# Kernel tuning notes

Measured on AMD Instinct MI355X. Metric: run time of the kernel, lower is better.

The kernel has to match this reference:

```python
import jax, jax.numpy as jnp
import numpy as np

UNITS = 128; NRBF = 10; MAXN = 3; MAXL = 3; SBF = MAXN * MAXL
NLAYERS = 3; CUTOFF = 5.0; TB_CUTOFF = 4.0; NELEM = 95
NTOTAL = 60000; NLOCAL = 50000; NGHOST = NTOTAL - NLOCAL
NEDGE = 250000; NTRIPLE = 1000000


def silu(x):
    return x * jax.nn.sigmoid(x)


def polynomial(r, cutoff):
    # smooth polynomial cutoff, zero beyond `cutoff`
    ratio = r / cutoff
    p = 1.0 - 6.0 * ratio**5 + 15.0 * ratio**4 - 10.0 * ratio**3
    return jnp.where(r <= cutoff, p, 0.0)


def rbf(r):  # [E] -> [E, NRBF] radial basis
    mu = jnp.linspace(0.0, CUTOFF, NRBF).astype(r.dtype)
    return jnp.exp(-((r[:, None] - mu) ** 2) / 0.5)


def sbf(r, theta):  # [T],[T] -> [T, SBF] radial x angular product basis
    n = jnp.arange(1, MAXN + 1, dtype=r.dtype)
    rad = jnp.sin(n * jnp.pi * r[:, None] / TB_CUTOFF) / (r[:, None] + 1e-6)  # [T,MAXN]
    l = jnp.arange(MAXL, dtype=r.dtype)
    ang = jnp.cos(l * theta[:, None])  # [T,MAXL]
    return (rad[:, :, None] * ang[:, None, :]).reshape(r.shape[0], SBF)


def setup_inputs() -> dict:
    key = jax.random.key(0)
    ks = jax.random.split(key, 40)
    w = lambda i, shape: 0.05 * jax.random.normal(ks[i], shape, dtype=jnp.float32)
    return {
        "atomic_numbers": jax.random.randint(ks[0], (NTOTAL,), 0, NELEM),
        "atom_pos": 10.0 * jax.random.uniform(ks[1], (NTOTAL, 3), dtype=jnp.float32),
        "cell": jax.random.normal(ks[2], (1, 3, 3), dtype=jnp.float32),
        "pbc_offsets": jnp.zeros((NEDGE, 3), jnp.float32),
        "edge_src": jax.random.randint(ks[3], (NEDGE,), 0, NLOCAL),
        "edge_dst": jax.random.randint(ks[4], (NEDGE,), 0, NTOTAL),
        "three_body_indices": jax.random.randint(ks[5], (NTRIPLE, 2), 0, NEDGE),
        "batch": jnp.zeros((NTOTAL,), jnp.int32),
        "ghost_map": jax.random.randint(ks[6], (NGHOST,), 0, NLOCAL),
        "nlocal": NLOCAL,
        "atom_embed_w": w(7, (NELEM, UNITS)),
        "edge_enc_w": w(8, (NRBF, UNITS)),
        "edge_enc_b": w(9, (UNITS,)),
        "tb_atom_w": w(10, (NLAYERS, UNITS, SBF)),
        "tb_atom_b": w(11, (NLAYERS, SBF)),
        "tb_gate_w": w(12, (NLAYERS, SBF, UNITS)),
        "tb_gate_b": w(13, (NLAYERS, UNITS)),
        "ge_wm": w(14, (NLAYERS, 3 * UNITS, UNITS)),
        "ge_bm": w(15, (NLAYERS, UNITS)),
        "ge_wg": w(16, (NLAYERS, 3 * UNITS, UNITS)),
        "ge_bg": w(17, (NLAYERS, UNITS)),
        "el_edge_w": w(18, (NLAYERS, NRBF, UNITS)),
        "el_edge_b": w(19, (NLAYERS, UNITS)),
        "ga_wm": w(20, (NLAYERS, 3 * UNITS, UNITS)),
        "ga_bm": w(21, (NLAYERS, UNITS)),
        "ga_wg": w(22, (NLAYERS, 3 * UNITS, UNITS)),
        "ga_bg": w(23, (NLAYERS, UNITS)),
        "el_atom_w": w(24, (NLAYERS, NRBF, UNITS)),
        "el_atom_b": w(25, (NLAYERS, UNITS)),
        "final_w1": w(26, (UNITS, UNITS)),
        "final_b1": w(27, (UNITS,)),
        "final_w2": w(28, (UNITS, 1)),
        "final_b2": w(29, (1,)),
        "e_scale": 1.0 + w(30, (NELEM,)),
        "e_shift": w(31, (NELEM,)),
    }


def m3gnet_forward(atom_pos, cell, pbc_offsets, atom_embed_w, edge_enc_w, edge_enc_b,
                   tb_atom_w, tb_atom_b, tb_gate_w, tb_gate_b,
                   ge_wm, ge_bm, ge_wg, ge_bg, el_edge_w, el_edge_b,
                   ga_wm, ga_bm, ga_wg, ga_bg, el_atom_w, el_atom_b,
                   final_w1, final_b1, final_w2, final_b2, e_scale, e_shift,
                   atomic_numbers, edge_src, edge_dst, three_body_indices, batch, ghost_map, nlocal):
    src, dst = edge_src, edge_dst
    edge_batch = batch[src]
    # geometry
    edge_vector = atom_pos[src] - (atom_pos[dst] + jnp.einsum('bi,bij->bj', pbc_offsets, cell[edge_batch]))
    edge_length = jnp.linalg.norm(edge_vector, axis=1)  # [E]
    ij = three_body_indices[:, 0]
    ik = three_body_indices[:, 1]
    vij, vik = edge_vector[ij], edge_vector[ik]
    rij, rik = edge_length[ij], edge_length[ik]
    cos_jik = jnp.clip(jnp.sum(vij * vik, axis=1) / (rij * rik + 1e-12), -1.0 + 1e-7, 1.0 - 1e-7)
    # embeddings / bases
    atom_attr = jax.nn.one_hot(atomic_numbers, NELEM, dtype=atom_embed_w.dtype) @ atom_embed_w  # [ntotal,U]
    edge_attr_zero = rbf(edge_length)  # [E,NRBF]
    edge_attr = edge_attr_zero @ edge_enc_w + edge_enc_b  # [E,U]
    three_basis = sbf(rik, jnp.arccos(cos_jik))  # [T,SBF]
    n_edges = edge_attr.shape[0]
    cut_ij = polynomial(edge_length[ij], TB_CUTOFF)[:, None]
    cut_ik = polynomial(edge_length[ik], TB_CUTOFF)[:, None]
    center_of_k = src[ik]  # center atom of edge k (< nlocal)
    for L in range(NLAYERS):
        if L > 0:
            # LammpsExchange: pad + fill ghost slots from mapped local atoms
            atom_attr = jnp.concatenate([atom_attr, atom_attr[ghost_map]], axis=0)
        # three-body interaction
        atom_mlp_out = jax.nn.sigmoid(atom_attr[:nlocal] @ tb_atom_w[L] + tb_atom_b[L])  # [nlocal,SBF]
        atom_mask = atom_mlp_out[center_of_k] * cut_ij * cut_ik  # [T,SBF]
        tb_masked = three_basis * atom_mask
        tb_out = jnp.zeros((n_edges, SBF), tb_masked.dtype).at[ij].add(tb_masked)
        edge_attr = edge_attr + (tb_out @ tb_gate_w[L] + tb_gate_b[L])
        # edge update: gated MLP on [h_src, h_dst, e]
        feat = jnp.concatenate([atom_attr[src], atom_attr[dst], edge_attr], axis=1)  # [E,3U]
        gmlp_e = silu(feat @ ge_wm[L] + ge_bm[L]) * jax.nn.sigmoid(feat @ ge_wg[L] + ge_bg[L])
        edge_attr = edge_attr + gmlp_e * (edge_attr_zero @ el_edge_w[L] + el_edge_b[L])
        # atom update: gated MLP + scatter-add to local centers
        feat = jnp.concatenate([atom_attr[src], atom_attr[dst], edge_attr], axis=1)
        ap = silu(feat @ ga_wm[L] + ga_bm[L]) * jax.nn.sigmoid(feat @ ga_wg[L] + ga_bg[L])
        ap = ap * (edge_attr_zero @ el_atom_w[L] + el_atom_b[L])
        agg = jnp.zeros((nlocal, UNITS), ap.dtype).at[src].add(ap)
        atom_attr = atom_attr[:nlocal] + agg  # truncate ghosts
    # readout on local atoms only
    e = (silu(atom_attr @ final_w1 + final_b1) @ final_w2 + final_b2).reshape(-1)
    z_local = atomic_numbers[:nlocal]
    e = e * e_scale[z_local] + e_shift[z_local]
    return jnp.sum(e)[None]  # [1]


def reference(atomic_numbers, atom_pos, cell, pbc_offsets, edge_src, edge_dst, three_body_indices,
              batch, ghost_map, nlocal, atom_embed_w, edge_enc_w, edge_enc_b,
              tb_atom_w, tb_atom_b, tb_gate_w, tb_gate_b,
              ge_wm, ge_bm, ge_wg, ge_bg, el_edge_w, el_edge_b,
              ga_wm, ga_bm, ga_wg, ga_bg, el_atom_w, el_atom_b,
              final_w1, final_b1, final_w2, final_b2, e_scale, e_shift):
    return m3gnet_forward(atom_pos, cell, pbc_offsets, atom_embed_w, edge_enc_w, edge_enc_b,
                          tb_atom_w, tb_atom_b, tb_gate_w, tb_gate_b,
                          ge_wm, ge_bm, ge_wg, ge_bg, el_edge_w, el_edge_b,
                          ga_wm, ga_bm, ga_wg, ga_bg, el_atom_w, el_atom_b,
                          final_w1, final_b1, final_w2, final_b2, e_scale, e_shift,
                          atomic_numbers, edge_src, edge_dst, three_body_indices, batch, ghost_map, nlocal)
```

## Files before the change

kernel.cpp:

```cpp
#include <hip/hip_runtime.h>
#include <math.h>

#define UNITS   128
#define NRBF    10
#define SBF     9
#define NLAYERS 3
#define NELEM   95
#define NTOTAL  60000
#define NLOCAL  50000
#define NGHOST  10000
#define NEDGE   250000
#define NTRIPLE 1000000
#define CUTOFF  5.0f
#define TBCUT   4.0f
#define PI_F    3.14159265358979323846f
#define FSTR    424
#define MEDGE   64
#define SCHUNK  1024
#define NCHUNK  ((NEDGE + SCHUNK - 1)/SCHUNK)

typedef __attribute__((ext_vector_type(8))) short short8;
typedef __attribute__((ext_vector_type(4))) float f32x4;

__device__ __forceinline__ float sigm(float x){ return 1.0f/(1.0f+__expf(-x)); }
__device__ __forceinline__ float polycut(float r){
    float q = r*(1.0f/TBCUT);
    float q2 = q*q, q3 = q2*q;
    float p = 1.0f - 6.0f*q2*q3 + 15.0f*q2*q2 - 10.0f*q3;
    return (r <= TBCUT) ? p : 0.0f;
}
__device__ __forceinline__ ushort f2bf(float x){
    unsigned u = __float_as_uint(x);
    unsigned r = (u + 0x7fffu + ((u>>16)&1u)) >> 16;
    return (ushort)r;
}
__device__ __forceinline__ float bf2f(ushort h){
    return __uint_as_float(((unsigned)h) << 16);
}
__device__ __forceinline__ f32x4 splat4(float x){ f32x4 v = {x,x,x,x}; return v; }
__device__ __forceinline__ float gatef(float xm, float xg){
    float d = (1.0f+__expf(-xm))*(1.0f+__expf(-xg));
    return xm*__builtin_amdgcn_rcpf(d);
}

__global__ void k_edge_geom(const float* __restrict__ pos, const float* __restrict__ cell,
                            const float* __restrict__ pbc, const int* __restrict__ src,
                            const int* __restrict__ dst, const int* __restrict__ batch,
                            float* __restrict__ evec, float* __restrict__ elen,
                            float* __restrict__ rbf0){
    int e = blockIdx.x*blockDim.x + threadIdx.x;
    if (e >= NEDGE) return;
    int s = src[e], d = dst[e];
    int b = batch[s];
    const float* C = cell + b*9;
    float p0 = pbc[e*3+0], p1 = pbc[e*3+1], p2 = pbc[e*3+2];
    float vx = pos[s*3+0] - (pos[d*3+0] + p0*C[0] + p1*C[3] + p2*C[6]);
    float vy = pos[s*3+1] - (pos[d*3+1] + p0*C[1] + p1*C[4] + p2*C[7]);
    float vz = pos[s*3+2] - (pos[d*3+2] + p0*C[2] + p1*C[5] + p2*C[8]);
    float r = sqrtf(vx*vx + vy*vy + vz*vz);
    evec[e*3+0] = vx; evec[e*3+1] = vy; evec[e*3+2] = vz;
    elen[e] = r;
    #pragma unroll
    for (int i = 0; i < NRBF; i++){
        float mu = (CUTOFF/(NRBF-1))*i;
        float dm = r - mu;
        rbf0[e*NRBF + i] = __expf(-dm*dm*2.0f);
    }
}

__global__ void k_embed(const int* __restrict__ anum, const float* __restrict__ embw,
                        ushort* __restrict__ Ah){
    int t = blockIdx.x*blockDim.x + threadIdx.x;
    if (t >= NTOTAL*32) return;
    int a = t >> 5, q = t & 31;
    float4 v = ((const float4*)embw)[anum[a]*32 + q];
    ushort4 h;
    h.x = f2bf(v.x); h.y = f2bf(v.y); h.z = f2bf(v.z); h.w = f2bf(v.w);
    ((ushort4*)Ah)[t] = h;
}

__global__ void k_pack_all(const float* __restrict__ gewm, const float* __restrict__ gewg,
                           const float* __restrict__ gawm, const float* __restrict__ gawg,
                           const float* __restrict__ tbg,  const float* __restrict__ encw,
                           const float* __restrict__ elew, const float* __restrict__ elaw,
                           const float* __restrict__ gebm, const float* __restrict__ gebg,
                           const float* __restrict__ tbb,  const float* __restrict__ encb,
                           ushort* __restrict__ wmain, ushort* __restrict__ wext,
                           ushort* __restrict__ waux,  ushort* __restrict__ wencb,
                           float* __restrict__ btot){
    int blk = blockIdx.x, tid = threadIdx.x;
    if (blk < 288){
        int t = blk*256 + tid;
        if (t >= 3*4*12*8*64) return;
        int lane = t & 63;
        int nt   = (t>>6) & 7;
        int rest = t >> 9;
        int kb   = rest % 12;
        int r2   = rest / 12;
        int mat  = r2 & 3;
        int L    = r2 >> 2;
        const float* src;
        if      (mat == 0) src = gewm;
        else if (mat == 1) src = gewg;
        else if (mat == 2) src = gawm;
        else               src = gawg;
        src += (size_t)L*384*128;
        int n = nt*16 + (lane & 15);
        int kbase = kb*32 + (lane>>4)*8;
        ushort* dst = wmain + (size_t)t*8;
        #pragma unroll
        for (int j = 0; j < 8; j++) dst[j] = f2bf(src[(size_t)(kbase+j)*128 + n]);
    } else if (blk < 300){
        int t = (blk-288)*256 + tid;
        if (t >= 3*2*512) return;
        int lane = t & 63;
        int nt   = (t>>6) & 7;
        int mat  = (t>>9) & 1;
        int L    = t >> 10;
        const float* W  = ((mat==0)? gewm : gewg) + (size_t)L*384*128;
        const float* tg = tbg + (size_t)L*SBF*UNITS;
        int n = nt*16 + (lane & 15);
        ushort* dst = wext + (size_t)t*8;
        #pragma unroll
        for (int j = 0; j < 8; j++){
            int k = (lane>>4)*8 + j;
            float v = 0.0f;
            if (k >= 10 && k <= 18){
                int s = k - 10;
                for (int kk = 0; kk < 128; kk++)
                    v = fmaf(tg[s*UNITS+kk], W[(size_t)(256+kk)*128 + n], v);
            } else if (k < 10 && L == 0){
                for (int kk = 0; kk < 128; kk++)
                    v = fmaf(encw[k*UNITS+kk], W[(size_t)(256+kk)*128 + n], v);
            }
            dst[j] = f2bf(v);
        }
    } else if (blk < 318){
        int t = (blk-300)*256 + tid;
        if (t >= 3*3*512) return;
        int lane = t & 63;
        int nt   = (t>>6) & 7;
        int rest = t >> 9;
        int mat  = rest % 3;
        int L    = rest / 3;
        int n = nt*16 + (lane & 15);
        ushort* dst = waux + (size_t)t*8;
        #pragma unroll
        for (int j = 0; j < 8; j++){
            int k = (lane>>4)*8 + j;
            float v = 0.0f;
            if (mat == 0){ if (k < 10) v = elew[(size_t)L*NRBF*UNITS + k*UNITS + n]; }
            else if (mat == 1){ if (k < 10) v = elaw[(size_t)L*NRBF*UNITS + k*UNITS + n]; }
            else { if (k >= 10 && k <= 18) v = tbg[(size_t)L*SBF*UNITS + (k-10)*UNITS + n]; }
            dst[j] = f2bf(v);
        }
    } else if (blk < 320){
        int t = (blk-318)*256 + tid;
        if (t >= 512) return;
        int lane = t & 63;
        int nt   = t >> 6;
        int n = nt*16 + (lane & 15);
        ushort* dst = wencb + (size_t)t*8;
        #pragma unroll
        for (int j = 0; j < 8; j++){
            int k = (lane>>4)*8 + j;
            float v = (k < 10) ? encw[k*UNITS + n] : 0.0f;
            dst[j] = f2bf(v);
        }
    } else {
        int t = (blk-320)*256 + tid;
        if (t >= 3*2*128) return;
        int n = t & 127;
        int mat = (t>>7) & 1;
        int L = t >> 8;
        const float* W = ((mat==0)? gewm : gewg) + (size_t)L*384*128;
        const float* be = ((mat==0)? gebm : gebg) + (size_t)L*UNITS;
        const float* tb = tbb + (size_t)L*UNITS;
        float v = be[n];
        for (int kk = 0; kk < 128; kk++){
            float f = tb[kk];
            if (L == 0) f += encb[kk];
            v = fmaf(f, W[(size_t)(256+kk)*128 + n], v);
        }
        btot[t] = v;
    }
}

template<int GATHER, int WAH>
__global__ void k_tb_mlp(const float* __restrict__ Fin, const int* __restrict__ anum,
                         const float* __restrict__ embw,
                         const float* __restrict__ W, const float* __restrict__ b,
                         float* __restrict__ out, float* __restrict__ aggOut,
                         ushort* __restrict__ Ah){
    int a = blockIdx.x*blockDim.x + threadIdx.x;
    if (a >= NLOCAL) return;
    float acc[SBF];
    #pragma unroll
    for (int s = 0; s < SBF; s++) acc[s] = b[s];
    const float4* row4 = GATHER ? (const float4*)(embw + (size_t)anum[a]*UNITS)
                                : (const float4*)(Fin + (size_t)a*UNITS);
    float4* agg4 = (float4*)(aggOut + (size_t)a*UNITS);
    ushort4* ah4 = (ushort4*)(Ah + (size_t)a*UNITS);
    for (int k4 = 0; k4 < 32; k4++){
        float4 v = row4[k4];
        agg4[k4] = v;
        if (WAH){
            ushort4 h;
            h.x = f2bf(v.x); h.y = f2bf(v.y); h.z = f2bf(v.z); h.w = f2bf(v.w);
            ah4[k4] = h;
        }
        const float* w = W + (k4*4)*SBF;
        #pragma unroll
        for (int s = 0; s < SBF; s++){
            acc[s] = fmaf(v.x, w[s],        acc[s]);
            acc[s] = fmaf(v.y, w[s+SBF],    acc[s]);
            acc[s] = fmaf(v.z, w[s+2*SBF],  acc[s]);
            acc[s] = fmaf(v.w, w[s+3*SBF],  acc[s]);
        }
    }
    #pragma unroll
    for (int s = 0; s < SBF; s++) out[a*SBF + s] = sigm(acc[s]);
}

__global__ void k_triple_pass1(const float* __restrict__ elen, const int* __restrict__ tbi,
                               int* __restrict__ cnt, int* __restrict__ u_ij,
                               int* __restrict__ u_ik, int* __restrict__ hist){
    int t = blockIdx.x*blockDim.x + threadIdx.x;
    int tc = min(t, NTRIPLE-1);
    int ij = tbi[2*tc], ik = tbi[2*tc+1];
    bool valid = (t < NTRIPLE) && (polycut(elen[ij])*polycut(elen[ik]) != 0.0f);

    __shared__ int wbase[4];
    __shared__ int gbase;
    int tid = threadIdx.x;
    int wid = tid >> 6, lid = tid & 63;
    unsigned long long m = __ballot(valid);
    int wpre = __popcll(m & ((1ull << lid) - 1ull));
    if (lid == 0) wbase[wid] = __popcll(m);
    __syncthreads();
    if (tid == 0){
        int s = 0;
        #pragma unroll
        for (int i = 0; i < 4; i++){ int v = wbase[i]; wbase[i] = s; s += v; }
        gbase = (s > 0) ? atomicAdd(cnt, s) : 0;
    }
    __syncthreads();
    if (valid){
        int idx = gbase + wbase[wid] + wpre;
        u_ij[idx] = ij;
        u_ik[idx] = ik;
        atomicAdd(&hist[ij], 1);
    }
}
__global__ void k_scanA(const int* __restrict__ hist, int* __restrict__ toff,
                        int* __restrict__ bsum){
    __shared__ int sh[256];
    int b = blockIdx.x, tid = threadIdx.x;
    int base = b*SCHUNK + tid*4;
    int v0 = 0, v1 = 0, v2 = 0, v3 = 0;
    if (base+0 < NEDGE) v0 = hist[base+0];
    if (base+1 < NEDGE) v1 = hist[base+1];
    if (base+2 < NEDGE) v2 = hist[base+2];
    if (base+3 < NEDGE) v3 = hist[base+3];
    int tsum = v0+v1+v2+v3;
    sh[tid] = tsum;
    __syncthreads();
    for (int off = 1; off < 256; off <<= 1){
        int x = (tid >= off) ? sh[tid-off] : 0;
        __syncthreads();
        sh[tid] += x;
        __syncthreads();
    }
    int run = (tid == 0) ? 0 : sh[tid-1];
    if (tid == 255) bsum[b] = sh[255];
    if (base+0 < NEDGE) toff[base+0] = run; run += v0;
    if (base+1 < NEDGE) toff[base+1] = run; run += v1;
    if (base+2 < NEDGE) toff[base+2] = run; run += v2;
    if (base+3 < NEDGE) toff[base+3] = run;
}
__global__ void k_scanB(int* __restrict__ bsum, int* __restrict__ total){
    __shared__ int sh[256];
    int tid = threadIdx.x;
    int v = (tid < NCHUNK) ? bsum[tid] : 0;
    sh[tid] = v;
    __syncthreads();
    for (int off = 1; off < 256; off <<= 1){
        int x = (tid >= off) ? sh[tid-off] : 0;
        __syncthreads();
        sh[tid] += x;
        __syncthreads();
    }
    if (tid < NCHUNK) bsum[tid] = sh[tid] - v;
    if (tid == 255) *total = sh[255];
}
__global__ void k_scanC(int* __restrict__ toff, int* __restrict__ curs,
                        const int* __restrict__ bsum, const int* __restrict__ total){
    int i = blockIdx.x*blockDim.x + threadIdx.x;
    if (i < NEDGE){
        int v = toff[i] + bsum[i/SCHUNK];
        toff[i] = v;
        curs[i] = v;
    }
    if (i == 0) toff[NEDGE] = *total;
}
__global__ void k_triple_pass2(const float* __restrict__ evec, const float* __restrict__ elen,
                               const int* __restrict__ esrc, const int* __restrict__ cnt,
                               const int* __restrict__ u_ij, const int* __restrict__ u_ik,
                               int* __restrict__ curs, int* __restrict__ t_ka,
                               float* __restrict__ t_cf){
    int n = *cnt;
    for (int t = blockIdx.x*blockDim.x + threadIdx.x; t < n; t += gridDim.x*blockDim.x){
        int ij = u_ij[t], ik = u_ik[t];
        float rij = elen[ij], rik = elen[ik];
        float cc = polycut(rij)*polycut(rik);
        float ax = evec[ij*3+0], ay = evec[ij*3+1], az = evec[ij*3+2];
        float bx = evec[ik*3+0], by = evec[ik*3+1], bz = evec[ik*3+2];
        float dot = ax*bx + ay*by + az*bz;
        float c = dot/(rij*rik + 1e-12f);
        c = fminf(fmaxf(c, -1.0f + 1e-7f), 1.0f - 1e-7f);
        float a0 = 1.0f, a1 = c, a2 = 2.0f*c*c - 1.0f;
        float x = rik*(PI_F/TBCUT);
        float s1, c1;
        __sincosf(x, &s1, &c1);
        float s2 = 2.0f*s1*c1;
        float s3 = s1*(3.0f - 4.0f*s1*s1);
        float inv = 1.0f/(rik + 1e-6f);
        float r0 = s1*inv, r1 = s2*inv, r2 = s3*inv;
        int pos = atomicAdd(&curs[ij], 1);
        t_ka[pos] = esrc[ik];
        float* d = t_cf + (size_t)pos*SBF;
        d[0] = r0*a0*cc; d[1] = r0*a1*cc; d[2] = r0*a2*cc;
        d[3] = r1*a0*cc; d[4] = r1*a1*cc; d[5] = r1*a2*cc;
        d[6] = r2*a0*cc; d[7] = r2*a1*cc; d[8] = r2*a2*cc;
    }
}

template<int ENC, int GM, int STORE>
__global__
void k_gated_fused(const ushort* __restrict__ Ah, const int* __restrict__ gmap,
                   ushort* __restrict__ Eh,
                   const int* __restrict__ esrc, const int* __restrict__ edst,
                   const float* __restrict__ rbf0,
                   const int* __restrict__ toff, const int* __restrict__ t_ka,
                   const float* __restrict__ t_cf, const float* __restrict__ amlp,
                   const ushort* __restrict__ Wem, const ushort* __restrict__ Weg,
                   const ushort* __restrict__ Wam, const ushort* __restrict__ Wag,
                   const ushort* __restrict__ WxM, const ushort* __restrict__ WxG,
                   const ushort* __restrict__ Ble, const ushort* __restrict__ Bla,
                   const ushort* __restrict__ Bte, const ushort* __restrict__ Benc,
                   const float* __restrict__ btm, const float* __restrict__ btg,
                   const float* __restrict__ bam, const float* __restrict__ bag,
                   const float* __restrict__ tbb, const float* __restrict__ eleb,
                   const float* __restrict__ elab, const float* __restrict__ encb,
                   float* __restrict__ agg){
    __shared__ __align__(16) ushort feat_s[MEDGE*FSTR];
    __shared__ int src_s[MEDGE];
    __shared__ int dst_s[MEDGE];

    const int tid = threadIdx.x;
    const int e0  = blockIdx.x*MEDGE;

    if (tid < MEDGE){
        int e = min(e0 + tid, NEDGE-1);
        src_s[tid] = esrc[e];
        int d = edst[e];
        if (GM && d >= NLOCAL) d = gmap[d - NLOCAL];
        dst_s[tid] = d;
    }
    __syncthreads();

    #pragma unroll
    for (int j = 0; j < 6; j++){
        int idx = j*512 + tid;
        int m   = idx/48;
        int k8  = idx - m*48;
        short8 h;
        if (k8 < 16){
            h = *(const short8*)(Ah + (size_t)src_s[m]*UNITS + k8*8);
        } else if (k8 < 32){
            h = *(const short8*)(Ah + (size_t)dst_s[m]*UNITS + (k8-16)*8);
        } else if (ENC){
            short8 z = {0,0,0,0,0,0,0,0};
            h = z;
        } else {
            int e = min(e0 + m, NEDGE-1);
            h = *(const short8*)(Eh + (size_t)e*UNITS + (k8-32)*8);
        }
        *(short8*)&feat_s[m*FSTR + k8*8] = h;
    }
    if (tid < MEDGE){
        int e = min(e0 + tid, NEDGE-1);
        float tb[SBF];
        #pragma unroll
        for (int s = 0; s < SBF; s++) tb[s] = 0.0f;
        int beg = toff[e], end = toff[e+1];
        for (int t = beg; t < end; t++){
            const float* cf = t_cf + (size_t)t*SBF;
            const float* am = amlp + (size_t)t_ka[t]*SBF;
            #pragma unroll
            for (int s = 0; s < SBF; s++) tb[s] = fmaf(cf[s], am[s], tb[s]);
        }
        ushort row[32];
        #pragma unroll
        for (int k = 0; k < 10; k++) row[k] = f2bf(rbf0[(size_t)e*NRBF + k]);
        #pragma unroll
        for (int s = 0; s < SBF; s++) row[10+s] = f2bf(tb[s]);
        #pragma unroll
        for (int k = 19; k < 32; k++) row[k] = 0;
        #pragma unroll
        for (int j8 = 0; j8 < 4; j8++)
            *(short8*)&feat_s[tid*FSTR + 384 + j8*8] = *(const short8*)&row[j8*8];
    }
    __syncthreads();

    const int lane = tid & 63;
    const int w    = tid >> 6;
    const int quad = lane >> 4;
    const int l15  = lane & 15;
    const int c    = w*16 + l15;

    f32x4 acc_em[4], acc_eg[4], acc_te[4], acc_le[4], acc_en[ENC ? 4 : 1];
    {
        float bm = btm[c], bg = btg[c], tb = tbb[c], le = eleb[c];
        #pragma unroll
        for (int mt = 0; mt < 4; mt++){
            acc_em[mt] = splat4(bm); acc_eg[mt] = splat4(bg);
            acc_te[mt] = splat4(tb); acc_le[mt] = splat4(le);
        }
        if (ENC){
            float eb = encb[c];
            #pragma unroll
            for (int mt = 0; mt < 4; mt++) acc_en[mt] = splat4(eb);
        }
    }
    const ushort* abase = feat_s + l15*FSTR + quad*8;

    for (int ks = 0; ks < 12; ks++){
        short8 a[4];
        #pragma unroll
        for (int mt = 0; mt < 4; mt++)
            a[mt] = *(const short8*)(abase + mt*16*FSTR + ks*32);
        size_t boff = ((size_t)(ks*8 + w)*64 + lane)*8;
        short8 b_em = *(const short8*)(Wem + boff);
        short8 b_eg = *(const short8*)(Weg + boff);
        #pragma unroll
        for (int mt = 0; mt < 4; mt++){
            acc_em[mt] = __builtin_amdgcn_mfma_f32_16x16x32_bf16(a[mt], b_em, acc_em[mt], 0, 0, 0);
            acc_eg[mt] = __builtin_amdgcn_mfma_f32_16x16x32_bf16(a[mt], b_eg, acc_eg[mt], 0, 0, 0);
        }
    }
    {
        size_t bx = ((size_t)w*64 + lane)*8;
        short8 b_xm = *(const short8*)(WxM + bx);
        short8 b_xg = *(const short8*)(WxG + bx);
        short8 b_te = *(const short8*)(Bte + bx);
        short8 b_le = *(const short8*)(Ble + bx);
        #pragma unroll
        for (int mt = 0; mt < 4; mt++){
            short8 ax = *(const short8*)(abase + mt*16*FSTR + 384);
            acc_em[mt] = __builtin_amdgcn_mfma_f32_16x16x32_bf16(ax, b_xm, acc_em[mt], 0, 0, 0);
            acc_eg[mt] = __builtin_amdgcn_mfma_f32_16x16x32_bf16(ax, b_xg, acc_eg[mt], 0, 0, 0);
            acc_te[mt] = __builtin_amdgcn_mfma_f32_16x16x32_bf16(ax, b_te, acc_te[mt], 0, 0, 0);
            acc_le[mt] = __builtin_amdgcn_mfma_f32_16x16x32_bf16(ax, b_le, acc_le[mt], 0, 0, 0);
        }
        if (ENC){
            short8 b_en = *(const short8*)(Benc + bx);
            #pragma unroll
            for (int mt = 0; mt < 4; mt++){
                short8 ax = *(const short8*)(abase + mt*16*FSTR + 384);
                acc_en[mt] = __builtin_amdgcn_mfma_f32_16x16x32_bf16(ax, b_en, acc_en[mt], 0, 0, 0);
            }
        }
    }

    __syncthreads();
    #pragma unroll
    for (int mt = 0; mt < 4; mt++){
        #pragma unroll
        for (int r = 0; r < 4; r++){
            int ml = mt*16 + quad*4 + r;
            int e  = e0 + ml;
            if (e >= NEDGE) continue;
            float gate = gatef(acc_em[mt][r], acc_eg[mt][r]);
            float eold = ENC ? acc_en[mt][r] : bf2f(feat_s[ml*FSTR + 256 + c]);
            float enew = eold + acc_te[mt][r] + gate*acc_le[mt][r];
            feat_s[ml*FSTR + 256 + c] = f2bf(enew);
        }
    }
    __syncthreads();

    if (STORE){
        #pragma unroll
        for (int j = 0; j < 2; j++){
            int idx = j*512 + tid;
            int row = idx >> 4;
            int q8  = idx & 15;
            int e   = e0 + row;
            if (e < NEDGE)
                *(short8*)(Eh + (size_t)e*UNITS + q8*8)
                    = *(const short8*)&feat_s[row*FSTR + 256 + q8*8];
        }
    }

    f32x4 acc_am[4], acc_ag[4], acc_la[4];
    {
        float bm = bam[c], bg = bag[c], lb = elab[c];
        #pragma unroll
        for (int mt = 0; mt < 4; mt++){
            acc_am[mt] = splat4(bm); acc_ag[mt] = splat4(bg); acc_la[mt] = splat4(lb);
        }
    }
    for (int ks = 0; ks < 12; ks++){
        short8 a[4];
        #pragma unroll
        for (int mt = 0; mt < 4; mt++)
            a[mt] = *(const short8*)(abase + mt*16*FSTR + ks*32);
        size_t boff = ((size_t)(ks*8 + w)*64 + lane)*8;
        short8 b_am = *(const short8*)(Wam + boff);
        short8 b_ag = *(const short8*)(Wag + boff);
        #pragma unroll
        for (int mt = 0; mt < 4; mt++){
            acc_am[mt] = __builtin_amdgcn_mfma_f32_16x16x32_bf16(a[mt], b_am, acc_am[mt], 0, 0, 0);
            acc_ag[mt] = __builtin_amdgcn_mfma_f32_16x16x32_bf16(a[mt], b_ag, acc_ag[mt], 0, 0, 0);
        }
    }
    {
        size_t bx = ((size_t)w*64 + lane)*8;
        short8 b_la = *(const short8*)(Bla + bx);
        #pragma unroll
        for (int mt = 0; mt < 4; mt++){
            short8 ax = *(const short8*)(abase + mt*16*FSTR + 384);
            acc_la[mt] = __builtin_amdgcn_mfma_f32_16x16x32_bf16(ax, b_la, acc_la[mt], 0, 0, 0);
        }
    }

    #pragma unroll
    for (int mt = 0; mt < 4; mt++){
        #pragma unroll
        for (int r = 0; r < 4; r++){
            int ml = mt*16 + quad*4 + r;
            int e  = e0 + ml;
            if (e >= NEDGE) continue;
            float gate = gatef(acc_am[mt][r], acc_ag[mt][r]);
            atomicAdd(&agg[(size_t)src_s[ml]*UNITS + c], gate*acc_la[mt][r]);
        }
    }
}

__global__ void k_final(const float* __restrict__ A, const float* __restrict__ W1,
                        const float* __restrict__ b1, const float* __restrict__ W2,
                        const float* __restrict__ b2, const int* __restrict__ anum,
                        const float* __restrict__ escl, const float* __restrict__ eshf,
                        float* __restrict__ out){
    __shared__ float red[256];
    const int tid  = threadIdx.x;
    const int c    = tid & 127;
    const int half = tid >> 7;
    float b1c = b1[c];
    float w2c = W2[c];
    float b2v = b2[0];
    float tpart = 0.0f;
    const int npairs = NLOCAL/2;
    for (int p = blockIdx.x; p < npairs; p += gridDim.x){
        int a = 2*p + half;
        const float* h = A + (size_t)a*UNITS;
        float acc = b1c;
        for (int k = 0; k < UNITS; k++)
            acc = fmaf(h[k], W1[k*UNITS + c], acc);
        float hid = acc/(1.0f+__expf(-acc));
        int z = anum[a];
        float sc = escl[z];
        tpart = fmaf(sc*hid, w2c, tpart);
        if (c == 0) tpart += sc*b2v + eshf[z];
    }
    red[tid] = tpart;
    __syncthreads();
    for (int s = 128; s > 0; s >>= 1){
        if (tid < s) red[tid] += red[tid + s];
        __syncthreads();
    }
    if (tid == 0) atomicAdd(out, red[0]);
}

extern "C" void kernel_launch(void* const* d_in, const int* in_sizes, int n_in,
                              void* d_out, int out_size, void* d_ws, size_t ws_size,
                              hipStream_t stream){
    const int*   anum  = (const int*)d_in[0];
    const float* pos   = (const float*)d_in[1];
    const float* cell  = (const float*)d_in[2];
    const float* pbc   = (const float*)d_in[3];
    const int*   esrc  = (const int*)d_in[4];
    const int*   edst  = (const int*)d_in[5];
    const int*   tbi   = (const int*)d_in[6];
    const int*   batch = (const int*)d_in[7];
    const int*   gmap  = (const int*)d_in[8];
    const float* embw  = (const float*)d_in[10];
    const float* encw  = (const float*)d_in[11];
    const float* encb  = (const float*)d_in[12];
    const float* tbaw  = (const float*)d_in[13];
    const float* tbab  = (const float*)d_in[14];
    const float* tbgw  = (const float*)d_in[15];
    const float* tbgb  = (const float*)d_in[16];
    const float* gewm  = (const float*)d_in[17];
    const float* gebm  = (const float*)d_in[18];
    const float* gewg  = (const float*)d_in[19];
    const float* gebg  = (const float*)d_in[20];
    const float* elew  = (const float*)d_in[21];
    const float* eleb  = (const float*)d_in[22];
    const float* gawm  = (const float*)d_in[23];
    const float* gabm  = (const float*)d_in[24];
    const float* gawg  = (const float*)d_in[25];
    const float* gabg  = (const float*)d_in[26];
    const float* elaw  = (const float*)d_in[27];
    const float* elab  = (const float*)d_in[28];
    const float* fw1   = (const float*)d_in[29];
    const float* fb1   = (const float*)d_in[30];
    const float* fw2   = (const float*)d_in[31];
    const float* fb2   = (const float*)d_in[32];
    const float* escl  = (const float*)d_in[33];
    const float* eshf  = (const float*)d_in[34];
    (void)in_sizes; (void)n_in; (void)out_size; (void)ws_size;

    float* ws     = (float*)d_ws;
    float* aggA   = ws;
    float* aggB   = aggA   + (size_t)NLOCAL*UNITS;
    float* evec   = aggB   + (size_t)NLOCAL*UNITS;
    float* elen   = evec   + (size_t)NEDGE*3;
    float* rbf0   = elen   + (size_t)NEDGE;
    float* amlp   = rbf0   + (size_t)NEDGE*NRBF;
    float* btot   = amlp   + (size_t)NLOCAL*SBF;
    int*   hist   = (int*)(btot + 3*2*128);
    int*   tcnt   = hist + NEDGE;
    int*   toff   = tcnt + 4;
    int*   curs   = toff + NEDGE + 1;
    int*   bsum   = curs + NEDGE + 3;
    int*   total  = bsum + NCHUNK + 1;
    int*   u_ij   = total + 4;
    int*   u_ik   = u_ij + NTRIPLE;
    int*   t_ka   = u_ik + NTRIPLE;
    float* t_cf   = (float*)(t_ka + NTRIPLE);
    ushort* edgeEh = (ushort*)(t_cf + (size_t)9*NTRIPLE);
    ushort* embedAh = edgeEh + (size_t)NEDGE*UNITS;
    ushort* aggAh   = embedAh + (size_t)NTOTAL*UNITS;
    ushort* wmain  = aggAh + (size_t)NLOCAL*UNITS;
    ushort* wext   = wmain + (size_t)3*4*49152;
    ushort* waux   = wext  + (size_t)3*2*4096;
    ushort* wencb  = waux  + (size_t)3*3*4096;

    float* out = (float*)d_out;
    hipMemsetAsync(out, 0, sizeof(float), stream);
    hipMemsetAsync(hist, 0, (NEDGE+4)*sizeof(int), stream);

    k_pack_all<<<323, 256, 0, stream>>>(gewm, gewg, gawm, gawg, tbgw, encw,
                                        elew, elaw, gebm, gebg, tbgb, encb,
                                        wmain, wext, waux, wencb, btot);
    k_edge_geom<<<(NEDGE+255)/256, 256, 0, stream>>>(pos, cell, pbc, esrc, edst, batch,
                                                     evec, elen, rbf0);
    k_embed<<<(NTOTAL*32+255)/256, 256, 0, stream>>>(anum, embw, embedAh);
    k_triple_pass1<<<(NTRIPLE+255)/256, 256, 0, stream>>>(elen, tbi, tcnt, u_ij, u_ik, hist);
    k_scanA<<<NCHUNK, 256, 0, stream>>>(hist, toff, bsum);
    k_scanB<<<1, 256, 0, stream>>>(bsum, total);
    k_scanC<<<(NEDGE+255)/256, 256, 0, stream>>>(toff, curs, bsum, total);
    k_triple_pass2<<<256, 256, 0, stream>>>(evec, elen, esrc, tcnt, u_ij, u_ik,
                                            curs, t_ka, t_cf);

    const int gemm_blocks = (NEDGE + MEDGE - 1)/MEDGE;
    float*  Fin[3]  = { nullptr, aggA, aggB };
    float*  Aout[3] = { aggA,    aggB, aggA };
    for (int L = 0; L < NLAYERS; L++){
        const ushort* wmL = wmain + (size_t)L*4*49152;
        const ushort* wxL = wext  + (size_t)L*2*4096;
        const ushort* waL = waux  + (size_t)L*3*4096;
        if (L == 0)
            k_tb_mlp<1,0><<<(NLOCAL+255)/256, 256, 0, stream>>>(nullptr, anum, embw,
                tbaw + (size_t)L*UNITS*SBF, tbab + (size_t)L*SBF, amlp, Aout[L], aggAh);
        else
            k_tb_mlp<0,1><<<(NLOCAL+255)/256, 256, 0, stream>>>(Fin[L], anum, embw,
                tbaw + (size_t)L*UNITS*SBF, tbab + (size_t)L*SBF, amlp, Aout[L], aggAh);
        const ushort* AhL = (L == 0) ? embedAh : aggAh;
        #define GATED_ARGS AhL, gmap, edgeEh, esrc, edst, rbf0, toff, t_ka, t_cf, amlp, \
            wmL + 0*49152, wmL + 1*49152, wmL + 2*49152, wmL + 3*49152, \
            wxL + 0*4096,  wxL + 1*4096, \
            waL + 0*4096,  waL + 1*4096, waL + 2*4096, wencb, \
            btot + (size_t)L*2*128, btot + (size_t)L*2*128 + 128, \
            gabm + (size_t)L*UNITS, gabg + (size_t)L*UNITS, \
            tbgb + (size_t)L*UNITS, eleb + (size_t)L*UNITS, elab + (size_t)L*UNITS, \
            encb, Aout[L]
        if (L == 0)
            k_gated_fused<1,0,1><<<gemm_blocks, 512, 0, stream>>>(GATED_ARGS);
        else if (L == 1)
            k_gated_fused<0,1,1><<<gemm_blocks, 512, 0, stream>>>(GATED_ARGS);
        else
            k_gated_fused<0,1,0><<<gemm_blocks, 512, 0, stream>>>(GATED_ARGS);
        #undef GATED_ARGS
    }
    k_final<<<1024, 256, 0, stream>>>(aggA, fw1, fb1, fw2, fb2, anum, escl, eshf, out);
}
```

Before: 1.172 ms.

## Fuse prologue kernels, merge scan passes, and move final MLP to MFMA

Merges weight packing, edge geometry and atom embedding into one prologue launch, and folds the block-sum scan into the first scan kernel using a last-block-done atomic. Rewrites the final readout MLP as a bf16 MFMA tile kernel over 64-atom blocks with a pre-packed W1, replacing the scalar per-atom loop. The goal is fewer launches and a faster final layer, at the cost of bf16 rounding in the readout and reliance on tcnt+1 being zeroed as the done counter.

Measured after the change: 1.000 ms. 1.17x faster.

```diff
diff --git a/kernel.cpp b/kernel.cpp
--- a/kernel.cpp
+++ b/kernel.cpp
@@ -19,6 +19,17 @@
 #define SCHUNK  1024
 #define NCHUNK  ((NEDGE + SCHUNK - 1)/SCHUNK)
 
+#define PB_MAIN 288
+#define PB_EXT  12
+#define PB_AUX  18
+#define PB_ENC  2
+#define PB_BIAS 3
+#define PB_W1   8
+#define PB_PACK (PB_MAIN+PB_EXT+PB_AUX+PB_ENC+PB_BIAS+PB_W1)
+#define PB_GEOM 977
+#define PB_EMB  7500
+#define PB_ALL  (PB_PACK+PB_GEOM+PB_EMB)
+
 typedef __attribute__((ext_vector_type(8))) short short8;
 typedef __attribute__((ext_vector_type(4))) float f32x4;
 
@@ -43,53 +54,24 @@
     return xm*__builtin_amdgcn_rcpf(d);
 }
 
-__global__ void k_edge_geom(const float* __restrict__ pos, const float* __restrict__ cell,
-                            const float* __restrict__ pbc, const int* __restrict__ src,
-                            const int* __restrict__ dst, const int* __restrict__ batch,
-                            float* __restrict__ evec, float* __restrict__ elen,
-                            float* __restrict__ rbf0){
-    int e = blockIdx.x*blockDim.x + threadIdx.x;
-    if (e >= NEDGE) return;
-    int s = src[e], d = dst[e];
-    int b = batch[s];
-    const float* C = cell + b*9;
-    float p0 = pbc[e*3+0], p1 = pbc[e*3+1], p2 = pbc[e*3+2];
-    float vx = pos[s*3+0] - (pos[d*3+0] + p0*C[0] + p1*C[3] + p2*C[6]);
-    float vy = pos[s*3+1] - (pos[d*3+1] + p0*C[1] + p1*C[4] + p2*C[7]);
-    float vz = pos[s*3+2] - (pos[d*3+2] + p0*C[2] + p1*C[5] + p2*C[8]);
-    float r = sqrtf(vx*vx + vy*vy + vz*vz);
-    evec[e*3+0] = vx; evec[e*3+1] = vy; evec[e*3+2] = vz;
-    elen[e] = r;
-    #pragma unroll
-    for (int i = 0; i < NRBF; i++){
-        float mu = (CUTOFF/(NRBF-1))*i;
-        float dm = r - mu;
-        rbf0[e*NRBF + i] = __expf(-dm*dm*2.0f);
-    }
-}
-
-__global__ void k_embed(const int* __restrict__ anum, const float* __restrict__ embw,
-                        ushort* __restrict__ Ah){
-    int t = blockIdx.x*blockDim.x + threadIdx.x;
-    if (t >= NTOTAL*32) return;
-    int a = t >> 5, q = t & 31;
-    float4 v = ((const float4*)embw)[anum[a]*32 + q];
-    ushort4 h;
-    h.x = f2bf(v.x); h.y = f2bf(v.y); h.z = f2bf(v.z); h.w = f2bf(v.w);
-    ((ushort4*)Ah)[t] = h;
-}
-
-__global__ void k_pack_all(const float* __restrict__ gewm, const float* __restrict__ gewg,
+__global__ void k_prologue(const float* __restrict__ gewm, const float* __restrict__ gewg,
                            const float* __restrict__ gawm, const float* __restrict__ gawg,
                            const float* __restrict__ tbg,  const float* __restrict__ encw,
                            const float* __restrict__ elew, const float* __restrict__ elaw,
                            const float* __restrict__ gebm, const float* __restrict__ gebg,
                            const float* __restrict__ tbb,  const float* __restrict__ encb,
+                           const float* __restrict__ fw1,
+                           const float* __restrict__ pos, const float* __restrict__ cell,
+                           const float* __restrict__ pbc, const int* __restrict__ esrc,
+                           const int* __restrict__ edst, const int* __restrict__ batch,
+                           const int* __restrict__ anum, const float* __restrict__ embw,
                            ushort* __restrict__ wmain, ushort* __restrict__ wext,
                            ushort* __restrict__ waux,  ushort* __restrict__ wencb,
-                           float* __restrict__ btot){
+                           ushort* __restrict__ wfin,  float* __restrict__ btot,
+                           float* __restrict__ evec, float* __restrict__ elen,
+                           float* __restrict__ rbf0, ushort* __restrict__ Ah){
     int blk = blockIdx.x, tid = threadIdx.x;
-    if (blk < 288){
+    if (blk < PB_MAIN){
         int t = blk*256 + tid;
         if (t >= 3*4*12*8*64) return;
         int lane = t & 63;
@@ -110,8 +92,8 @@
         ushort* dst = wmain + (size_t)t*8;
         #pragma unroll
         for (int j = 0; j < 8; j++) dst[j] = f2bf(src[(size_t)(kbase+j)*128 + n]);
-    } else if (blk < 300){
-        int t = (blk-288)*256 + tid;
+    } else if (blk < PB_MAIN+PB_EXT){
+        int t = (blk-PB_MAIN)*256 + tid;
         if (t >= 3*2*512) return;
         int lane = t & 63;
         int nt   = (t>>6) & 7;
@@ -135,8 +117,8 @@
             }
             dst[j] = f2bf(v);
         }
-    } else if (blk < 318){
-        int t = (blk-300)*256 + tid;
+    } else if (blk < PB_MAIN+PB_EXT+PB_AUX){
+        int t = (blk-PB_MAIN-PB_EXT)*256 + tid;
         if (t >= 3*3*512) return;
         int lane = t & 63;
         int nt   = (t>>6) & 7;
@@ -154,8 +136,8 @@
             else { if (k >= 10 && k <= 18) v = tbg[(size_t)L*SBF*UNITS + (k-10)*UNITS + n]; }
             dst[j] = f2bf(v);
         }
-    } else if (blk < 320){
-        int t = (blk-318)*256 + tid;
+    } else if (blk < PB_MAIN+PB_EXT+PB_AUX+PB_ENC){
+        int t = (blk-PB_MAIN-PB_EXT-PB_AUX)*256 + tid;
         if (t >= 512) return;
         int lane = t & 63;
         int nt   = t >> 6;
@@ -167,8 +149,8 @@
             float v = (k < 10) ? encw[k*UNITS + n] : 0.0f;
             dst[j] = f2bf(v);
         }
-    } else {
-        int t = (blk-320)*256 + tid;
+    } else if (blk < PB_MAIN+PB_EXT+PB_AUX+PB_ENC+PB_BIAS){
+        int t = (blk-PB_MAIN-PB_EXT-PB_AUX-PB_ENC)*256 + tid;
         if (t >= 3*2*128) return;
         int n = t & 127;
         int mat = (t>>7) & 1;
@@ -183,6 +165,44 @@
             v = fmaf(f, W[(size_t)(256+kk)*128 + n], v);
         }
         btot[t] = v;
+    } else if (blk < PB_PACK){
+        int t = (blk-PB_MAIN-PB_EXT-PB_AUX-PB_ENC-PB_BIAS)*256 + tid;
+        if (t >= 4*8*64) return;
+        int lane = t & 63;
+        int nt   = (t>>6) & 7;
+        int kb   = t >> 9;
+        int n = nt*16 + (lane & 15);
+        int kbase = kb*32 + (lane>>4)*8;
+        ushort* dst = wfin + (size_t)t*8;
+        #pragma unroll
+        for (int j = 0; j < 8; j++) dst[j] = f2bf(fw1[(size_t)(kbase+j)*128 + n]);
+    } else if (blk < PB_PACK+PB_GEOM){
+        int e = (blk-PB_PACK)*256 + tid;
+        if (e >= NEDGE) return;
+        int s = esrc[e], d = edst[e];
+        int b = batch[s];
+        const float* C = cell + b*9;
+        float p0 = pbc[e*3+0], p1 = pbc[e*3+1], p2 = pbc[e*3+2];
+        float vx = pos[s*3+0] - (pos[d*3+0] + p0*C[0] + p1*C[3] + p2*C[6]);
+        float vy = pos[s*3+1] - (pos[d*3+1] + p0*C[1] + p1*C[4] + p2*C[7]);
+        float vz = pos[s*3+2] - (pos[d*3+2] + p0*C[2] + p1*C[5] + p2*C[8]);
+        float r = sqrtf(vx*vx + vy*vy + vz*vz);
+        evec[e*3+0] = vx; evec[e*3+1] = vy; evec[e*3+2] = vz;
+        elen[e] = r;
+        #pragma unroll
+        for (int i = 0; i < NRBF; i++){
+            float mu = (CUTOFF/(NRBF-1))*i;
+            float dm = r - mu;
+            rbf0[e*NRBF + i] = __expf(-dm*dm*2.0f);
+        }
+    } else {
+        int t = (blk-PB_PACK-PB_GEOM)*256 + tid;
+        if (t >= NTOTAL*32) return;
+        int a = t >> 5, q = t & 31;
+        float4 v = ((const float4*)embw)[anum[a]*32 + q];
+        ushort4 h;
+        h.x = f2bf(v.x); h.y = f2bf(v.y); h.z = f2bf(v.z); h.w = f2bf(v.w);
+        ((ushort4*)Ah)[t] = h;
     }
 }
 
@@ -252,9 +272,11 @@
         atomicAdd(&hist[ij], 1);
     }
 }
-__global__ void k_scanA(const int* __restrict__ hist, int* __restrict__ toff,
-                        int* __restrict__ bsum){
+__global__ void k_scanAB(const int* __restrict__ hist, int* __restrict__ toff,
+                         int* __restrict__ bsum, int* __restrict__ total,
+                         int* __restrict__ done){
     __shared__ int sh[256];
+    __shared__ int amlast;
     int b = blockIdx.x, tid = threadIdx.x;
     int base = b*SCHUNK + tid*4;
     int v0 = 0, v1 = 0, v2 = 0, v3 = 0;
@@ -272,26 +294,31 @@
         __syncthreads();
     }
     int run = (tid == 0) ? 0 : sh[tid-1];
-    if (tid == 255) bsum[b] = sh[255];
     if (base+0 < NEDGE) toff[base+0] = run; run += v0;
     if (base+1 < NEDGE) toff[base+1] = run; run += v1;
     if (base+2 < NEDGE) toff[base+2] = run; run += v2;
     if (base+3 < NEDGE) toff[base+3] = run;
-}
-__global__ void k_scanB(int* __restrict__ bsum, int* __restrict__ total){
-    __shared__ int sh[256];
-    int tid = threadIdx.x;
-    int v = (tid < NCHUNK) ? bsum[tid] : 0;
-    sh[tid] = v;
-    __syncthreads();
-    for (int off = 1; off < 256; off <<= 1){
-        int x = (tid >= off) ? sh[tid-off] : 0;
+    if (tid == 255){
+        bsum[b] = sh[255];
+        __threadfence();
+        amlast = (atomicAdd(done, 1) == gridDim.x - 1);
+    }
+    __syncthreads();
+    if (amlast){
+        __threadfence();
+        int v = (tid < NCHUNK) ? bsum[tid] : 0;
         __syncthreads();
-        sh[tid] += x;
+        sh[tid] = v;
         __syncthreads();
-    }
-    if (tid < NCHUNK) bsum[tid] = sh[tid] - v;
-    if (tid == 255) *total = sh[255];
+        for (int off = 1; off < 256; off <<= 1){
+            int x = (tid >= off) ? sh[tid-off] : 0;
+            __syncthreads();
+            sh[tid] += x;
+            __syncthreads();
+        }
+        if (tid < NCHUNK) bsum[tid] = sh[tid] - v;
+        if (tid == 255) *total = sh[255];
+    }
 }
 __global__ void k_scanC(int* __restrict__ toff, int* __restrict__ curs,
                         const int* __restrict__ bsum, const int* __restrict__ total){
@@ -547,39 +574,95 @@
     }
 }
 
-__global__ void k_final(const float* __restrict__ A, const float* __restrict__ W1,
+__global__ void k_final(const float* __restrict__ A, const ushort* __restrict__ Wf,
                         const float* __restrict__ b1, const float* __restrict__ W2,
                         const float* __restrict__ b2, const int* __restrict__ anum,
                         const float* __restrict__ escl, const float* __restrict__ eshf,
                         float* __restrict__ out){
-    __shared__ float red[256];
-    const int tid  = threadIdx.x;
-    const int c    = tid & 127;
-    const int half = tid >> 7;
-    float b1c = b1[c];
+    __shared__ __align__(16) ushort a_s[64*136];
+    __shared__ float osum[64][8];
+    const int tid = threadIdx.x;
+    const int a0  = blockIdx.x*64;
+
+    #pragma unroll
+    for (int j = 0; j < 2; j++){
+        int idx = j*512 + tid;
+        int row = idx >> 4;
+        int q8  = idx & 15;
+        int a   = a0 + row;
+        short8 h;
+        if (a < NLOCAL){
+            const float4* p = (const float4*)(A + (size_t)a*UNITS + q8*8);
+            float4 v0 = p[0], v1 = p[1];
+            h[0] = (short)f2bf(v0.x); h[1] = (short)f2bf(v0.y);
+            h[2] = (short)f2bf(v0.z); h[3] = (short)f2bf(v0.w);
+            h[4] = (short)f2bf(v1.x); h[5] = (short)f2bf(v1.y);
+            h[6] = (short)f2bf(v1.z); h[7] = (short)f2bf(v1.w);
+        } else {
+            short8 z = {0,0,0,0,0,0,0,0};
+            h = z;
+        }
+        *(short8*)&a_s[row*136 + q8*8] = h;
+    }
+    __syncthreads();
+
+    const int lane = tid & 63;
+    const int w    = tid >> 6;
+    const int quad = lane >> 4;
+    const int l15  = lane & 15;
+    const int c    = w*16 + l15;
+
+    f32x4 acc[4];
+    {
+        float bc = b1[c];
+        #pragma unroll
+        for (int mt = 0; mt < 4; mt++) acc[mt] = splat4(bc);
+    }
+    const ushort* abase = a_s + l15*136 + quad*8;
+    for (int ks = 0; ks < 4; ks++){
+        size_t boff = ((size_t)(ks*8 + w)*64 + lane)*8;
+        short8 b = *(const short8*)(Wf + boff);
+        #pragma unroll
+        for (int mt = 0; mt < 4; mt++){
+            short8 a = *(const short8*)(abase + mt*16*136 + ks*32);
+            acc[mt] = __builtin_amdgcn_mfma_f32_16x16x32_bf16(a, b, acc[mt], 0, 0, 0);
+        }
+    }
     float w2c = W2[c];
-    float b2v = b2[0];
-    float tpart = 0.0f;
-    const int npairs = NLOCAL/2;
-    for (int p = blockIdx.x; p < npairs; p += gridDim.x){
-        int a = 2*p + half;
-        const float* h = A + (size_t)a*UNITS;
-        float acc = b1c;
-        for (int k = 0; k < UNITS; k++)
-            acc = fmaf(h[k], W1[k*UNITS + c], acc);
-        float hid = acc/(1.0f+__expf(-acc));
-        int z = anum[a];
-        float sc = escl[z];
-        tpart = fmaf(sc*hid, w2c, tpart);
-        if (c == 0) tpart += sc*b2v + eshf[z];
-    }
-    red[tid] = tpart;
-    __syncthreads();
-    for (int s = 128; s > 0; s >>= 1){
-        if (tid < s) red[tid] += red[tid + s];
-        __syncthreads();
-    }
-    if (tid == 0) atomicAdd(out, red[0]);
+    #pragma unroll
+    for (int mt = 0; mt < 4; mt++){
+        #pragma unroll
+        for (int r = 0; r < 4; r++){
+            int row = mt*16 + quad*4 + r;
+            float tot = acc[mt][r];
+            float hid = tot/(1.0f+__expf(-tot));
+            float v = hid*w2c;
+            v += __shfl_xor(v, 1);
+            v += __shfl_xor(v, 2);
+            v += __shfl_xor(v, 4);
+            v += __shfl_xor(v, 8);
+            if (l15 == 0) osum[row][w] = v;
+        }
+    }
+    __syncthreads();
+    if (tid < 64){
+        int a = a0 + tid;
+        float s = 0.0f;
+        #pragma unroll
+        for (int ww = 0; ww < 8; ww++) s += osum[tid][ww];
+        float part = 0.0f;
+        if (a < NLOCAL){
+            int z = anum[a];
+            part = escl[z]*(s + b2[0]) + eshf[z];
+        }
+        part += __shfl_xor(part, 1);
+        part += __shfl_xor(part, 2);
+        part += __shfl_xor(part, 4);
+        part += __shfl_xor(part, 8);
+        part += __shfl_xor(part, 16);
+        part += __shfl_xor(part, 32);
+        if (tid == 0) atomicAdd(out, part);
+    }
 }
 
 extern "C" void kernel_launch(void* const* d_in, const int* in_sizes, int n_in,
@@ -646,20 +729,19 @@
     ushort* wext   = wmain + (size_t)3*4*49152;
     ushort* waux   = wext  + (size_t)3*2*4096;
     ushort* wencb  = waux  + (size_t)3*3*4096;
+    ushort* wfin   = wencb + 4096;
 
     float* out = (float*)d_out;
     hipMemsetAsync(out, 0, sizeof(float), stream);
     hipMemsetAsync(hist, 0, (NEDGE+4)*sizeof(int), stream);
 
-    k_pack_all<<<323, 256, 0, stream>>>(gewm, gewg, gawm, gawg, tbgw, encw,
-                                        elew, elaw, gebm, gebg, tbgb, encb,
-                                        wmain, wext, waux, wencb, btot);
-    k_edge_geom<<<(NEDGE+255)/256, 256, 0, stream>>>(pos, cell, pbc, esrc, edst, batch,
-                                                     evec, elen, rbf0);
-    k_embed<<<(NTOTAL*32+255)/256, 256, 0, stream>>>(anum, embw, embedAh);
+    k_prologue<<<PB_ALL, 256, 0, stream>>>(gewm, gewg, gawm, gawg, tbgw, encw,
+                                           elew, elaw, gebm, gebg, tbgb, encb, fw1,
+                                           pos, cell, pbc, esrc, edst, batch, anum, embw,
+                                           wmain, wext, waux, wencb, wfin, btot,
+                                           evec, elen, rbf0, embedAh);
     k_triple_pass1<<<(NTRIPLE+255)/256, 256, 0, stream>>>(elen, tbi, tcnt, u_ij, u_ik, hist);
-    k_scanA<<<NCHUNK, 256, 0, stream>>>(hist, toff, bsum);
-    k_scanB<<<1, 256, 0, stream>>>(bsum, total);
+    k_scanAB<<<NCHUNK, 256, 0, stream>>>(hist, toff, bsum, total, tcnt+1);
     k_scanC<<<(NEDGE+255)/256, 256, 0, stream>>>(toff, curs, bsum, total);
     k_triple_pass2<<<256, 256, 0, stream>>>(evec, elen, esrc, tcnt, u_ij, u_ik,
                                             curs, t_ka, t_cf);
@@ -694,5 +776,6 @@
             k_gated_fused<0,1,0><<<gemm_blocks, 512, 0, stream>>>(GATED_ARGS);
         #undef GATED_ARGS
     }
-    k_final<<<1024, 256, 0, stream>>>(aggA, fw1, fb1, fw2, fb2, anum, escl, eshf, out);
-}
+    k_final<<<(NLOCAL+63)/64, 512, 0, stream>>>(aggA, wfin, fb1, fw2, fb2,
+                                                anum, escl, eshf, out);
+}
```
